# Performance work log

Hardware: AMD Instinct MI355X
Metric: run time of the kernel (lower is better)

## Reference

```python
import jax, jax.numpy as jnp
import numpy as np

N = 100000       # nodes
E = 1000000      # edges
IN = 128         # in_dim
HID = 64         # hid_dim
NET = 4          # n_etypes
STEPS = 5        # n_steps
G = 128          # graphs in batch
LBL = 10         # num_labels


def setup_inputs() -> dict:
    key = jax.random.key(0)
    ks = jax.random.split(key, 20)
    def w(k, shape, fan_in):
        return jax.random.normal(k, shape, jnp.float32) / np.sqrt(fan_in)
    return dict(
        x=jax.random.normal(ks[0], (N, IN), jnp.float32),
        src=jax.random.randint(ks[1], (E,), 0, N),
        dst=jax.random.randint(ks[2], (E,), 0, N),
        etype=jax.random.randint(ks[3], (E,), 0, NET),
        node2graph=jnp.sort(jax.random.randint(ks[4], (N,), 0, G)),
        # linear_in
        W_in=w(ks[5], (HID, IN), IN), b_in=jnp.zeros((HID,), jnp.float32),
        # per-edge-type linears [n_etypes, out, in]
        We=w(ks[6], (NET, HID, HID), HID), be=jnp.zeros((NET, HID), jnp.float32),
        # GRUCell (torch layout: rows = [r; z; n])
        W_ih=w(ks[7], (3 * HID, HID), HID), b_ih=jnp.zeros((3 * HID,), jnp.float32),
        W_hh=w(ks[8], (3 * HID, HID), HID), b_hh=jnp.zeros((3 * HID,), jnp.float32),
        # classifier
        W1=w(ks[9], (HID // 2, HID), HID), b1=jnp.zeros((HID // 2,), jnp.float32),
        W2=w(ks[10], (LBL, HID // 2), HID // 2), b2=jnp.zeros((LBL,), jnp.float32),
    )


def reference(x, W_in, b_in, We, be, W_ih, b_ih, W_hh, b_hh, W1, b1, W2, b2,
              src, dst, etype, node2graph):
    h = x @ W_in.T + b_in                                  # [N, HID]
    for _ in range(STEPS):
        # per-etype linear on node states: trans[e] = h @ We[e].T + be[e]
        trans = jnp.einsum('nd,efd->enf', h, We) + be[:, None, :]  # [NET, N, HID]
        msgs = trans[etype, src]                           # [E, HID] gather per edge
        a = jax.ops.segment_sum(msgs, dst, num_segments=N)  # scatter-add aggregation
        # GRUCell(a, h)
        gi = a @ W_ih.T + b_ih
        gh = h @ W_hh.T + b_hh
        ir, iz, i_n = jnp.split(gi, 3, axis=-1)
        hr, hz, h_n = jnp.split(gh, 3, axis=-1)
        r = jax.nn.sigmoid(ir + hr)
        z = jax.nn.sigmoid(iz + hz)
        n = jnp.tanh(i_n + r * h_n)
        h = (1.0 - z) * n + z * h
    # dgl.mean_nodes: per-graph mean of node states
    cnt = jnp.maximum(jax.ops.segment_sum(jnp.ones((N,), h.dtype), node2graph, num_segments=G), 1.0)
    hg = jax.ops.segment_sum(h, node2graph, num_segments=G) / cnt[:, None]  # [G, HID]
    return jax.nn.relu(hg @ W1.T + b1) @ W2.T + b2         # [G, LBL]
```

## Files before the change

### kernel.cpp

```cpp
#include <hip/hip_runtime.h>
#include <hip/hip_bf16.h>
#include <math.h>

#define N_NODES 100000
#define N_EDGES 1000000
#define IN_DIM 128
#define HID 64
#define NET 4
#define STEPS 5
#define G_GRAPHS 128
#define LBL 10
#define NGRP 6250
#define NGRP_PAD 6256
#define NBKT 1024
#define TILE_E 8192

typedef __attribute__((ext_vector_type(8))) short short8;
typedef __attribute__((ext_vector_type(4))) float f32x4;
typedef unsigned short ushort_t;

__device__ inline ushort_t f2bf(float v) {
    __hip_bfloat16 b = __float2bfloat16(v);
    return __builtin_bit_cast(ushort_t, b);
}
__device__ inline float bf2f(ushort_t u) {
    __hip_bfloat16 b = __builtin_bit_cast(__hip_bfloat16, u);
    return __bfloat162float(b);
}


__global__ void k_pack_b1(const float* __restrict__ We, const float* __restrict__ be,
                          ushort_t* __restrict__ B1, float* __restrict__ bs1) {
    int idx = blockIdx.x * blockDim.x + threadIdx.x;
    if (idx >= 6 * 16 * 4 * 16 * 8) return;
    int j = idx & 7, u = (idx >> 3) & 15, g = (idx >> 7) & 3, ct = (idx >> 9) & 15, s = idx >> 13;
    int m = ct * 16 + u;
    int t = m >> 6, o = m & 63;
    int sk = (s < 2) ? s : (s < 4) ? (s - 2) : (s - 4);
    int k = sk * 32 + g * 8 + j;
    float val = We[t * 4096 + o * 64 + k];
    ushort_t hi = f2bf(val);
    B1[idx] = (s < 4) ? hi : f2bf(val - bf2f(hi));
    if (s == 0 && g == 0 && j == 0) bs1[m] = be[t * 64 + o];
}

__global__ void k_pack_b2(const float* __restrict__ W_ih, const float* __restrict__ b_ih,
                          const float* __restrict__ W_hh, const float* __restrict__ b_hh,
                          ushort_t* __restrict__ B2, float* __restrict__ bg2) {
    int idx = blockIdx.x * blockDim.x + threadIdx.x;
    if (idx >= 12 * 16 * 4 * 16 * 8) return;
    int j = idx & 7, u = (idx >> 3) & 15, g = (idx >> 7) & 3, ct = (idx >> 9) & 15, s = idx >> 13;
    int m = ct * 16 + u;
    int q = m >> 6, gate = (m >> 4) & 3, c = q * 16 + (m & 15);
    int k = (s & 3) * 32 + g * 8 + j;
    float val;
    if (gate == 0)      { int jr = c;        val = (k < 64) ? W_ih[jr * 64 + k] : W_hh[jr * 64 + k - 64]; }
    else if (gate == 1) { int jr = 64 + c;   val = (k < 64) ? W_ih[jr * 64 + k] : W_hh[jr * 64 + k - 64]; }
    else if (gate == 2) { int jr = 128 + c;  val = (k < 64) ? W_ih[jr * 64 + k] : 0.f; }
    else                { int jr = 128 + c;  val = (k < 64) ? 0.f : W_hh[jr * 64 + k - 64]; }
    ushort_t hi = f2bf(val);
    B2[idx] = (s < 8) ? hi : f2bf(val - bf2f(hi));
    if (s == 0 && g == 0 && j == 0) {
        float bv;
        if (gate == 0)      bv = b_ih[c] + b_hh[c];
        else if (gate == 1) bv = b_ih[64 + c] + b_hh[64 + c];
        else if (gate == 2) bv = b_ih[128 + c];
        else                bv = b_hh[128 + c];
        bg2[m] = bv;
    }
}

__global__ void k_pack_bin(const float* __restrict__ W_in, ushort_t* __restrict__ BIN) {
    int idx = blockIdx.x * blockDim.x + threadIdx.x;
    if (idx >= 24576) return;
    int j = idx & 7, lu = (idx >> 3) & 63, ct = (idx >> 9) & 3, s = idx >> 11;
    int g = lu >> 4, u = lu & 15;
    int m = ct * 16 + u;
    int k = (s & 3) * 32 + g * 8 + j;
    float val = W_in[m * 128 + k];
    ushort_t hi = f2bf(val);
    BIN[idx] = (s < 8) ? hi : f2bf(val - bf2f(hi));
}

__global__ __launch_bounds__(256) void k_linear_in(const float* __restrict__ x,
        const ushort_t* __restrict__ BIN, const float* __restrict__ b_in,
        ushort_t* __restrict__ AH) {
    __shared__ float hlds[4][16 * 68];
    int tid = threadIdx.x;
    int lane = tid & 63, wp = tid >> 6;
    int g = lane >> 4, u = lane & 15;
    int grp = blockIdx.x * 4 + wp;
    bool ok = grp < NGRP;
    int row = ok ? (grp * 16 + u) : 0;
    short8 xhi[4], xlo[4];
    #pragma unroll
    for (int ks = 0; ks < 4; ++ks) {
        const float* xp = &x[(size_t)row * 128 + ks * 32 + g * 8];
        float4 v0 = ok ? *(const float4*)xp : make_float4(0.f, 0.f, 0.f, 0.f);
        float4 v1 = ok ? *(const float4*)(xp + 4) : make_float4(0.f, 0.f, 0.f, 0.f);
        float vv[8] = {v0.x, v0.y, v0.z, v0.w, v1.x, v1.y, v1.z, v1.w};
        #pragma unroll
        for (int j = 0; j < 8; ++j) {
            ushort_t hh = f2bf(vv[j]);
            xhi[ks][j] = (short)hh;
            xlo[ks][j] = (short)f2bf(vv[j] - bf2f(hh));
        }
    }
    f32x4 zero = {0.f, 0.f, 0.f, 0.f};
    f32x4 acc[4] = {zero, zero, zero, zero};
    #pragma unroll
    for (int s = 0; s < 12; ++s) {
        int ks = s & 3;
        short8 af = (s < 4) ? xhi[ks] : (s < 8) ? xlo[ks] : xhi[ks];
        #pragma unroll
        for (int ct = 0; ct < 4; ++ct) {
            short8 bf = *(const short8*)&BIN[((size_t)(s * 4 + ct) * 64 + lane) * 8];
            acc[ct] = __builtin_amdgcn_mfma_f32_16x16x32_bf16(af, bf, acc[ct], 0, 0, 0);
        }
    }
    #pragma unroll
    for (int ct = 0; ct < 4; ++ct) {
        float bo = b_in[ct * 16 + u];
        #pragma unroll
        for (int j = 0; j < 4; ++j)
            hlds[wp][(g * 4 + j) * 68 + ct * 16 + u] = acc[ct][j] + bo;
    }
    __syncthreads();
    #pragma unroll
    for (int k = 0; k < 4; ++k) {
        int bi = g + 4 * k;
        short8 ov;
        #pragma unroll
        for (int j = 0; j < 8; ++j) {
            float v = hlds[wp][u * 68 + (bi & 7) * 8 + j];
            ushort_t hh = f2bf(v);
            ov[j] = (bi < 8) ? (short)hh : (short)f2bf(v - bf2f(hh));
        }
        int blk = (bi < 8) ? (8 + bi) : (24 + (bi - 8));
        if (ok) *(short8*)&AH[((size_t)grp * 32 + blk) * 128 + u * 8] = ov;
    }
}


__global__ __launch_bounds__(256) void k_bhist(const int* __restrict__ dst,
        int* __restrict__ bhist) {
    __shared__ int h[NBKT];
    for (int i = threadIdx.x; i < NBKT; i += 256) h[i] = 0;
    __syncthreads();
    int idx = blockIdx.x * 256 + threadIdx.x;
    for (int e = idx; e < N_EDGES; e += 256 * 256) atomicAdd(&h[dst[e] >> 7], 1);
    __syncthreads();
    for (int i = threadIdx.x; i < NBKT; i += 256) {
        int c = h[i];
        if (c) atomicAdd(&bhist[i], c);
    }
}

__global__ __launch_bounds__(1024) void k_bscan(const int* __restrict__ bhist,
        int* __restrict__ bbase, int* __restrict__ bcursor) {
    __shared__ int ts[NBKT];
    int t = threadIdx.x;
    int v = bhist[t];
    ts[t] = v;
    __syncthreads();
    for (int off = 1; off < NBKT; off <<= 1) {
        int u = (t >= off) ? ts[t - off] : 0;
        __syncthreads();
        ts[t] += u;
        __syncthreads();
    }
    int excl = ts[t] - v;
    bbase[t] = excl;
    bcursor[t] = excl;
    if (t == NBKT - 1) bbase[NBKT] = ts[NBKT - 1];
}

__global__ __launch_bounds__(512) void k_bscatter(const int* __restrict__ src,
        const int* __restrict__ dst, const int* __restrict__ et,
        int* __restrict__ bcursor, unsigned int* __restrict__ ebuf) {
    __shared__ int hcnt[NBKT], loff[NBKT], gpos[NBKT], ps[512];
    __shared__ unsigned int stage[TILE_E];
    __shared__ unsigned short sbkt[TILE_E];
    int tid = threadIdx.x;
    int base = blockIdx.x * TILE_E;
    int tilecnt = min(TILE_E, N_EDGES - base);
    for (int i = tid; i < NBKT; i += 512) hcnt[i] = 0;
    __syncthreads();
    #pragma unroll
    for (int k = 0; k < TILE_E / 512; ++k) {
        int e = base + tid + k * 512;
        if (e < N_EDGES) atomicAdd(&hcnt[dst[e] >> 7], 1);
    }
    __syncthreads();
    int c0 = hcnt[tid * 2], c1 = hcnt[tid * 2 + 1];
    ps[tid] = c0 + c1;
    __syncthreads();
    for (int off = 1; off < 512; off <<= 1) {
        int u = (tid >= off) ? ps[tid - off] : 0;
        __syncthreads();
        ps[tid] += u;
        __syncthreads();
    }
    int ex = ps[tid] - (c0 + c1);
    loff[tid * 2] = ex;
    loff[tid * 2 + 1] = ex + c0;
    for (int b = tid; b < NBKT; b += 512) {
        int c = hcnt[b];
        gpos[b] = c ? atomicAdd(&bcursor[b], c) : 0;
    }
    __syncthreads();
    for (int i = tid; i < NBKT; i += 512) hcnt[i] = 0;
    __syncthreads();
    #pragma unroll
    for (int k = 0; k < TILE_E / 512; ++k) {
        int e = base + tid + k * 512;
        if (e < N_EDGES) {
            int d = dst[e];
            int b = d >> 7;
            int r = atomicAdd(&hcnt[b], 1);
            int lp = loff[b] + r;
            stage[lp] = (unsigned int)src[e] | ((unsigned int)et[e] << 20)
                      | ((unsigned int)(d & 127) << 22);
            sbkt[lp] = (unsigned short)b;
        }
    }
    __syncthreads();
    for (int i = tid; i < tilecnt; i += 512) {
        int b = sbkt[i];
        ebuf[gpos[b] + (i - loff[b])] = stage[i];
    }
}

__global__ __launch_bounds__(256) void k_bcsr(const unsigned int* __restrict__ ebuf,
        const int* __restrict__ bbase, int* __restrict__ adj, int* __restrict__ row_ptr) {
    __shared__ int ncnt[128], noff[129], nps[128];
    int b = blockIdx.x;
    int tid = threadIdx.x;
    int ebeg = bbase[b], eend = bbase[b + 1];
    int ecnt = eend - ebeg;
    if (tid < 128) ncnt[tid] = 0;
    __syncthreads();
    for (int i = tid; i < ecnt; i += 256) atomicAdd(&ncnt[(ebuf[ebeg + i] >> 22) & 127], 1);
    __syncthreads();
    int v = (tid < 128) ? ncnt[tid] : 0;
    if (tid < 128) nps[tid] = v;
    __syncthreads();
    for (int off = 1; off < 128; off <<= 1) {
        int u = (tid >= off && tid < 128) ? nps[tid - off] : 0;
        __syncthreads();
        if (tid < 128) nps[tid] += u;
        __syncthreads();
    }
    if (tid < 128) noff[tid] = nps[tid] - v;
    if (tid == 127) noff[128] = nps[127];
    __syncthreads();
    if (tid < 128) ncnt[tid] = 0;
    __syncthreads();
    for (int i = tid; i < ecnt; i += 256) {
        unsigned int p = ebuf[ebeg + i];
        int nl = (p >> 22) & 127;
        int r = atomicAdd(&ncnt[nl], 1);
        adj[ebeg + noff[nl] + r] = (int)(p & 0x3FFFFF);
    }
    for (int i = tid; i <= 128; i += 256) {
        int n = b * 128 + i;
        if (n <= N_NODES) row_ptr[n] = ebeg + noff[i];
    }
}

__global__ __launch_bounds__(512) void k_mm1(const ushort_t* __restrict__ AH,
        const ushort_t* __restrict__ B1, const float* __restrict__ bs1,
        ushort_t* __restrict__ trans) {
    __shared__ ushort_t lds[16896];
    int tid = threadIdx.x;
    size_t gb = (size_t)blockIdx.x * 8;
    #pragma unroll
    for (int it = 0; it < 4; ++it) {
        int f = it * 512 + tid;
        int gl = f >> 8, part = (f >> 7) & 1, inner = f & 127;
        size_t srcp = ((gb + gl) * 32 + (part ? 24 : 8)) * 128 + (size_t)inner * 8;
        *(short8*)&lds[f * 8] = *(const short8*)&AH[srcp];
    }
    __syncthreads();
    int lane = tid & 63, wp = tid >> 6;
    int q = wp & 3, rp = wp >> 2;
    int g = lane >> 4, u = lane & 15;
    int n0 = blockIdx.x * 128;
    f32x4 zero = {0.f, 0.f, 0.f, 0.f};
    f32x4 acc[4][4];
    #pragma unroll
    for (int i = 0; i < 4; ++i)
        #pragma unroll
        for (int j = 0; j < 4; ++j) acc[i][j] = zero;
    #pragma unroll
    for (int s = 0; s < 6; ++s) {
        int part = (s == 2 || s == 3) ? 1 : 0;
        int lb = ((s & 1) ? 4 : 0) + g;
        short8 bfr[4], afr[4];
        #pragma unroll
        for (int ct = 0; ct < 4; ++ct)
            bfr[ct] = *(const short8*)&B1[((size_t)(s * 16 + q * 4 + ct) * 64 + g * 16 + u) * 8];
        #pragma unroll
        for (int rt = 0; rt < 4; ++rt) {
            int gl = rp * 4 + rt;
            afr[rt] = *(const short8*)&lds[((gl * 2 + part) * 8 + lb) * 128 + u * 8];
        }
        #pragma unroll
        for (int rt = 0; rt < 4; ++rt)
            #pragma unroll
            for (int ct = 0; ct < 4; ++ct)
                acc[rt][ct] = __builtin_amdgcn_mfma_f32_16x16x32_bf16(afr[rt], bfr[ct], acc[rt][ct], 0, 0, 0);
    }
    float bsv[4];
    #pragma unroll
    for (int ct = 0; ct < 4; ++ct) bsv[ct] = bs1[q * 64 + ct * 16 + u];
    #pragma unroll
    for (int h = 0; h < 2; ++h) {
        __syncthreads();
        if (rp == h) {
            #pragma unroll
            for (int rt = 0; rt < 4; ++rt)
                #pragma unroll
                for (int ct = 0; ct < 4; ++ct)
                    #pragma unroll
                    for (int j = 0; j < 4; ++j) {
                        int rl = rt * 16 + g * 4 + j;
                        lds[rl * 264 + q * 64 + ct * 16 + u] = f2bf(acc[rt][ct][j] + bsv[ct]);
                    }
        }
        __syncthreads();
        int rl = tid >> 3, seg = tid & 7;
        int n = n0 + h * 64 + rl;
        if (n < N_NODES) {
            #pragma unroll
            for (int i = 0; i < 4; ++i) {
                short8 v = *(const short8*)&lds[rl * 264 + seg * 32 + i * 8];
                *(short8*)&trans[(size_t)n * 256 + seg * 32 + i * 8] = v;
            }
        }
    }
}

__global__ __launch_bounds__(512) void k_mm2(ushort_t* __restrict__ AH,
        const ushort_t* __restrict__ B2, const float* __restrict__ bg2) {
    __shared__ ushort_t lds[32768];
    int tid = threadIdx.x;
    size_t base = (size_t)blockIdx.x * 8 * 4096;
    #pragma unroll
    for (int it = 0; it < 8; ++it) {
        int f = it * 512 + tid;
        *(short8*)&lds[f * 8] = *(const short8*)&AH[base + (size_t)f * 8];
    }
    __syncthreads();
    int lane = tid & 63, wp = tid >> 6;
    int q = wp & 3, rp = wp >> 2;
    int g = lane >> 4, u = lane & 15;
    f32x4 zero = {0.f, 0.f, 0.f, 0.f};
    f32x4 acc[4][4];
    #pragma unroll
    for (int i = 0; i < 4; ++i)
        #pragma unroll
        for (int j = 0; j < 4; ++j) acc[i][j] = zero;
    const int bb2[12] = {0, 4, 8, 12, 16, 20, 24, 28, 0, 4, 8, 12};
    #pragma unroll
    for (int s = 0; s < 12; ++s) {
        short8 bfr[4], afr[4];
        #pragma unroll
        for (int ct = 0; ct < 4; ++ct)
            bfr[ct] = *(const short8*)&B2[((size_t)(s * 16 + q * 4 + ct) * 64 + g * 16 + u) * 8];
        #pragma unroll
        for (int rt = 0; rt < 4; ++rt) {
            int gl = rp * 4 + rt;
            afr[rt] = *(const short8*)&lds[(gl * 32 + bb2[s] + g) * 128 + u * 8];
        }
        #pragma unroll
        for (int rt = 0; rt < 4; ++rt)
            #pragma unroll
            for (int ct = 0; ct < 4; ++ct)
                acc[rt][ct] = __builtin_amdgcn_mfma_f32_16x16x32_bf16(afr[rt], bfr[ct], acc[rt][ct], 0, 0, 0);
    }
    __syncthreads();
    float bgv[4];
    #pragma unroll
    for (int ct = 0; ct < 4; ++ct) bgv[ct] = bg2[q * 64 + ct * 16 + u];
    int hid = q * 16 + u;
    int bhi = 8 + (hid >> 3), blo = 24 + (hid >> 3), el = hid & 7;
    #pragma unroll
    for (int rt = 0; rt < 4; ++rt) {
        int gl = rp * 4 + rt;
        #pragma unroll
        for (int j = 0; j < 4; ++j) {
            int uu = g * 4 + j;
            int shi = (gl * 32 + bhi) * 128 + uu * 8 + el;
            int slo = (gl * 32 + blo) * 128 + uu * 8 + el;
            float ho = bf2f(lds[shi]) + bf2f(lds[slo]);
            float rs  = acc[rt][0][j] + bgv[0];
            float zs  = acc[rt][1][j] + bgv[1];
            float inn = acc[rt][2][j] + bgv[2];
            float hnn = acc[rt][3][j] + bgv[3];
            float r = 1.f / (1.f + __expf(-rs));
            float z = 1.f / (1.f + __expf(-zs));
            float t = inn + r * hnn;
            float e2 = __expf(2.f * t);
            float nn = 1.f - 2.f / (e2 + 1.f);
            float hnew = (1.f - z) * nn + z * ho;
            ushort_t hh = f2bf(hnew);
            lds[shi] = hh;
            lds[slo] = f2bf(hnew - bf2f(hh));
        }
    }
    __syncthreads();
    #pragma unroll
    for (int it = 0; it < 4; ++it) {
        int c = it * 512 + tid;
        int gl = c >> 8, r = c & 255, bi = r >> 4, uu = r & 15;
        int blk = (bi < 8) ? (8 + bi) : (16 + bi);
        int lofs = (gl * 32 + blk) * 128 + uu * 8;
        short8 v = *(const short8*)&lds[lofs];
        *(short8*)&AH[base + (size_t)lofs] = v;
    }
}

__global__ __launch_bounds__(1024) void k_aggregate(const int* __restrict__ row_ptr,
        const int* __restrict__ adj, const ushort_t* __restrict__ trans,
        ushort_t* __restrict__ AH) {
    __shared__ float alds[16 * 72];
    int w = threadIdx.x >> 6, lane = threadIdx.x & 63;
    int grp = blockIdx.x;
    int n = grp * 16 + w;
    int beg = row_ptr[n], end = row_ptr[n + 1];
    float a0 = 0.f, a1 = 0.f, a2 = 0.f, a3 = 0.f;
    int i = beg;
    for (; i + 8 <= end; i += 8) {
        int pk[8];
        #pragma unroll
        for (int t = 0; t < 8; ++t) pk[t] = adj[i + t];
        float v[8];
        #pragma unroll
        for (int t = 0; t < 8; ++t)
            v[t] = bf2f(trans[(size_t)(pk[t] & 0xFFFFF) * 256 + (pk[t] >> 20) * 64 + lane]);
        a0 += v[0] + v[4]; a1 += v[1] + v[5]; a2 += v[2] + v[6]; a3 += v[3] + v[7];
    }
    for (; i + 2 <= end; i += 2) {
        int pk0 = adj[i], pk1 = adj[i + 1];
        a0 += bf2f(trans[(size_t)(pk0 & 0xFFFFF) * 256 + (pk0 >> 20) * 64 + lane]);
        a1 += bf2f(trans[(size_t)(pk1 & 0xFFFFF) * 256 + (pk1 >> 20) * 64 + lane]);
    }
    if (i < end) {
        int pk = adj[i];
        a2 += bf2f(trans[(size_t)(pk & 0xFFFFF) * 256 + (pk >> 20) * 64 + lane]);
    }
    alds[w * 72 + lane] = (a0 + a1) + (a2 + a3);
    __syncthreads();
    if (threadIdx.x < 256) {
        int bi = threadIdx.x >> 4, u = threadIdx.x & 15;
        int b8 = bi & 7;
        bool ishi = bi < 8;
        short8 ov;
        #pragma unroll
        for (int j = 0; j < 8; ++j) {
            float v = alds[u * 72 + b8 * 8 + j];
            ushort_t hh = f2bf(v);
            ov[j] = ishi ? (short)hh : (short)f2bf(v - bf2f(hh));
        }
        *(short8*)&AH[((size_t)grp * 32 + (ishi ? b8 : 16 + b8)) * 128 + u * 8] = ov;
    }
}

__global__ __launch_bounds__(256) void k_pool(const int* __restrict__ n2g,
        const ushort_t* __restrict__ AH, float* __restrict__ hg) {
    int gidx = blockIdx.x;
    int lo = 0, hi = N_NODES;
    while (lo < hi) { int mid = (lo + hi) >> 1; if (n2g[mid] < gidx) lo = mid + 1; else hi = mid; }
    int s = lo;
    hi = N_NODES;
    while (lo < hi) { int mid = (lo + hi) >> 1; if (n2g[mid] < gidx + 1) lo = mid + 1; else hi = mid; }
    int e = lo;
    int w = threadIdx.x >> 6, lane = threadIdx.x & 63;
    int bh = 8 + (lane >> 3), bl = 24 + (lane >> 3), el = lane & 7;
    float sum = 0.f;
    for (int n = s + w; n < e; n += 4) {
        size_t base = (size_t)(n >> 4) * 4096 + (size_t)(n & 15) * 8;
        sum += bf2f(AH[base + bh * 128 + el]) + bf2f(AH[base + bl * 128 + el]);
    }
    __shared__ float red[4][64];
    red[w][lane] = sum;
    __syncthreads();
    if (threadIdx.x < 64) {
        float tot = red[0][lane] + red[1][lane] + red[2][lane] + red[3][lane];
        float cnt = (float)(e - s);
        hg[gidx * 64 + lane] = tot / fmaxf(cnt, 1.f);
    }
}

__global__ __launch_bounds__(64) void k_cls(const float* __restrict__ hg,
        const float* __restrict__ W1, const float* __restrict__ b1,
        const float* __restrict__ W2, const float* __restrict__ b2,
        float* __restrict__ out) {
    int gidx = blockIdx.x;
    __shared__ float v[64];
    __shared__ float m[32];
    v[threadIdx.x] = hg[gidx * 64 + threadIdx.x];
    __syncthreads();
    if (threadIdx.x < 32) {
        float a = b1[threadIdx.x];
        #pragma unroll 8
        for (int k = 0; k < 64; ++k) a = fmaf(v[k], W1[threadIdx.x * 64 + k], a);
        m[threadIdx.x] = fmaxf(a, 0.f);
    }
    __syncthreads();
    if (threadIdx.x < 10) {
        float a = b2[threadIdx.x];
        #pragma unroll
        for (int j = 0; j < 32; ++j) a = fmaf(m[j], W2[threadIdx.x * 32 + j], a);
        out[gidx * 10 + threadIdx.x] = a;
    }
}

extern "C" void kernel_launch(void* const* d_in, const int* in_sizes, int n_in,
                              void* d_out, int out_size, void* d_ws, size_t ws_size,
                              hipStream_t stream) {
    const float* x    = (const float*)d_in[0];
    const int* src    = (const int*)d_in[1];
    const int* dst    = (const int*)d_in[2];
    const int* etype  = (const int*)d_in[3];
    const int* n2g    = (const int*)d_in[4];
    const float* W_in = (const float*)d_in[5];
    const float* b_in = (const float*)d_in[6];
    const float* We   = (const float*)d_in[7];
    const float* be   = (const float*)d_in[8];
    const float* W_ih = (const float*)d_in[9];
    const float* b_ih = (const float*)d_in[10];
    const float* W_hh = (const float*)d_in[11];
    const float* b_hh = (const float*)d_in[12];
    const float* W1   = (const float*)d_in[13];
    const float* b1   = (const float*)d_in[14];
    const float* W2   = (const float*)d_in[15];
    const float* b2   = (const float*)d_in[16];
    float* out = (float*)d_out;

    char* wsb = (char*)d_ws;
    size_t off = 0;
    auto alloc = [&](size_t bytes) -> void* {
        void* p = wsb + off;
        off += (bytes + 255) & ~(size_t)255;
        return p;
    };
    ushort_t* AH      = (ushort_t*)alloc((size_t)NGRP_PAD * 4096 * 2);
    ushort_t* trans   = (ushort_t*)alloc((size_t)N_NODES * 256 * 2);
    int*      adj     = (int*)     alloc((size_t)N_EDGES * 4);
    unsigned int* ebuf = (unsigned int*)alloc((size_t)N_EDGES * 4);
    int*      row_ptr = (int*)     alloc((size_t)(N_NODES + 1) * 4);
    int*      bhist   = (int*)     alloc((size_t)NBKT * 4);
    int*      bbase   = (int*)     alloc((size_t)(NBKT + 1) * 4);
    int*      bcursor = (int*)     alloc((size_t)NBKT * 4);
    ushort_t* B1      = (ushort_t*)alloc((size_t)6 * 16 * 4 * 16 * 8 * 2);
    float*    bs1     = (float*)   alloc(256 * 4);
    ushort_t* B2      = (ushort_t*)alloc((size_t)12 * 16 * 4 * 16 * 8 * 2);
    float*    bg2     = (float*)   alloc(256 * 4);
    ushort_t* BIN     = (ushort_t*)alloc((size_t)24576 * 2);
    float*    hg      = (float*)   alloc(128 * 64 * 4);

    hipMemsetAsync(AH + (size_t)NGRP * 4096, 0, (size_t)(NGRP_PAD - NGRP) * 4096 * 2, stream);

    hipLaunchKernelGGL(k_pack_b1, dim3(192), dim3(256), 0, stream, We, be, B1, bs1);
    hipLaunchKernelGGL(k_pack_b2, dim3(384), dim3(256), 0, stream, W_ih, b_ih, W_hh, b_hh, B2, bg2);
    hipLaunchKernelGGL(k_pack_bin, dim3(96), dim3(256), 0, stream, W_in, BIN);
    hipLaunchKernelGGL(k_linear_in, dim3((NGRP + 3) / 4), dim3(256), 0, stream, x, BIN, b_in, AH);

    hipMemsetAsync(bhist, 0, (size_t)NBKT * 4, stream);
    hipLaunchKernelGGL(k_bhist, dim3(256), dim3(256), 0, stream, dst, bhist);
    hipLaunchKernelGGL(k_bscan, dim3(1), dim3(1024), 0, stream, bhist, bbase, bcursor);
    hipLaunchKernelGGL(k_bscatter, dim3((N_EDGES + TILE_E - 1) / TILE_E), dim3(512), 0, stream,
                       src, dst, etype, bcursor, ebuf);
    hipLaunchKernelGGL(k_bcsr, dim3(NBKT), dim3(256), 0, stream, ebuf, bbase, adj, row_ptr);

    int gblk = NGRP_PAD / 8;
    for (int step = 0; step < STEPS; ++step) {
        hipLaunchKernelGGL(k_mm1, dim3(gblk), dim3(512), 0, stream, AH, B1, bs1, trans);
        hipLaunchKernelGGL(k_aggregate, dim3(NGRP), dim3(1024), 0, stream, row_ptr, adj, trans, AH);
        hipLaunchKernelGGL(k_mm2, dim3(gblk), dim3(512), 0, stream, AH, B2, bg2);
    }
    hipLaunchKernelGGL(k_pool, dim3(G_GRAPHS), dim3(256), 0, stream, n2g, AH, hg);
    hipLaunchKernelGGL(k_cls, dim3(G_GRAPHS), dim3(64), 0, stream, hg, W1, b1, W2, b2, out);
}
```

Baseline: 877.0 us.

## Aggregate raw node states per edge type, then apply edge linear after aggregation

Reorders the math: instead of computing per-etype transformed states for every node and gathering them, each step gathers bf16 hidden rows into four per-etype sums plus counts, then applies the edge-type weights and count-weighted bias with MFMA. The edge gather, edge matmul and GRU matmul are fused into one kernel per step, with ping-pong row-major hidden buffers. This removes the 256-wide trans buffer and two launches per step, and shrinks gather traffic to 64 values per edge. In exchange each block holds four accumulators per lane, uses a large LDS footprint, and gathers only the bf16 high part of h, which lowers precision.

```diff
diff --git a/kernel.cpp b/kernel.cpp
--- a/kernel.cpp
+++ b/kernel.cpp
@@ -29,19 +29,18 @@
 }
 
 
-__global__ void k_pack_b1(const float* __restrict__ We, const float* __restrict__ be,
-                          ushort_t* __restrict__ B1, float* __restrict__ bs1) {
+__global__ void k_pack_bc(const float* __restrict__ We, ushort_t* __restrict__ BC) {
     int idx = blockIdx.x * blockDim.x + threadIdx.x;
-    if (idx >= 6 * 16 * 4 * 16 * 8) return;
-    int j = idx & 7, u = (idx >> 3) & 15, g = (idx >> 7) & 3, ct = (idx >> 9) & 15, s = idx >> 13;
-    int m = ct * 16 + u;
-    int t = m >> 6, o = m & 63;
-    int sk = (s < 2) ? s : (s < 4) ? (s - 2) : (s - 4);
-    int k = sk * 32 + g * 8 + j;
-    float val = We[t * 4096 + o * 64 + k];
+    if (idx >= 24 * 4 * 64 * 8) return;
+    int j = idx & 7, lane = (idx >> 3) & 63, ct = (idx >> 9) & 3, sl = idx >> 11;
+    int g = lane >> 4, u = lane & 15;
+    int p = sl >> 3, ks = sl & 7;
+    int k = ks * 32 + g * 8 + j;
+    int t = k >> 6, d = k & 63;
+    int o = ct * 16 + u;
+    float val = We[t * 4096 + o * 64 + d];
     ushort_t hi = f2bf(val);
-    B1[idx] = (s < 4) ? hi : f2bf(val - bf2f(hi));
-    if (s == 0 && g == 0 && j == 0) bs1[m] = be[t * 64 + o];
+    BC[idx] = (p < 2) ? hi : f2bf(val - bf2f(hi));
 }
 
 __global__ void k_pack_b2(const float* __restrict__ W_ih, const float* __restrict__ b_ih,
@@ -84,7 +83,7 @@
 
 __global__ __launch_bounds__(256) void k_linear_in(const float* __restrict__ x,
         const ushort_t* __restrict__ BIN, const float* __restrict__ b_in,
-        ushort_t* __restrict__ AH) {
+        ushort_t* __restrict__ AH, ushort_t* __restrict__ hrow) {
     __shared__ float hlds[4][16 * 68];
     int tid = threadIdx.x;
     int lane = tid & 63, wp = tid >> 6;
@@ -137,10 +136,13 @@
             ov[j] = (bi < 8) ? (short)hh : (short)f2bf(v - bf2f(hh));
         }
         int blk = (bi < 8) ? (8 + bi) : (24 + (bi - 8));
-        if (ok) *(short8*)&AH[((size_t)grp * 32 + blk) * 128 + u * 8] = ov;
-    }
-}
-
+        if (ok) {
+            *(short8*)&AH[((size_t)grp * 32 + blk) * 128 + u * 8] = ov;
+            if (bi < 8)
+                *(short8*)&hrow[((size_t)(grp * 16 + u)) * 64 + bi * 8] = ov;
+        }
+    }
+}
 
 __global__ __launch_bounds__(256) void k_bhist(const int* __restrict__ dst,
         int* __restrict__ bhist) {
@@ -268,202 +270,207 @@
     }
 }
 
-__global__ __launch_bounds__(512) void k_mm1(const ushort_t* __restrict__ AH,
-        const ushort_t* __restrict__ B1, const float* __restrict__ bs1,
-        ushort_t* __restrict__ trans) {
-    __shared__ ushort_t lds[16896];
-    int tid = threadIdx.x;
-    size_t gb = (size_t)blockIdx.x * 8;
-    #pragma unroll
-    for (int it = 0; it < 4; ++it) {
-        int f = it * 512 + tid;
-        int gl = f >> 8, part = (f >> 7) & 1, inner = f & 127;
-        size_t srcp = ((gb + gl) * 32 + (part ? 24 : 8)) * 128 + (size_t)inner * 8;
-        *(short8*)&lds[f * 8] = *(const short8*)&AH[srcp];
-    }
-    __syncthreads();
-    int lane = tid & 63, wp = tid >> 6;
-    int q = wp & 3, rp = wp >> 2;
+__global__ __launch_bounds__(512) void k_step(const int* __restrict__ row_ptr,
+        const int* __restrict__ adj, const ushort_t* __restrict__ hin,
+        ushort_t* __restrict__ hout, ushort_t* __restrict__ AH,
+        const ushort_t* __restrict__ BC, const float* __restrict__ be,
+        const ushort_t* __restrict__ B2, const float* __restrict__ bg2) {
+    __shared__ float smem[16896];
+    float* aggf = smem;
+    float* cnts = smem + 16640;
+    ushort_t* als  = (ushort_t*)smem;
+    ushort_t* hlds = (ushort_t*)((char*)smem + 17408);
+
+    int tid = threadIdx.x, lane = tid & 63, wp = tid >> 6;
     int g = lane >> 4, u = lane & 15;
-    int n0 = blockIdx.x * 128;
+    int grp0 = blockIdx.x * 4;
+    int nbase = grp0 * 16;
+
+    #pragma unroll 1
+    for (int r = 0; r < 8; ++r) {
+        int nl = wp * 8 + r;
+        int n = nbase + nl;
+        float a0 = 0.f, a1 = 0.f, a2 = 0.f, a3 = 0.f;
+        float c0 = 0.f, c1 = 0.f, c2 = 0.f, c3 = 0.f;
+        if (n < N_NODES) {
+            int beg = row_ptr[n], end = row_ptr[n + 1];
+            int i = beg;
+            for (; i + 4 <= end; i += 4) {
+                int p0 = adj[i], p1 = adj[i + 1], p2 = adj[i + 2], p3 = adj[i + 3];
+                float v0 = bf2f(hin[(size_t)(p0 & 0xFFFFF) * 64 + lane]);
+                float v1 = bf2f(hin[(size_t)(p1 & 0xFFFFF) * 64 + lane]);
+                float v2 = bf2f(hin[(size_t)(p2 & 0xFFFFF) * 64 + lane]);
+                float v3 = bf2f(hin[(size_t)(p3 & 0xFFFFF) * 64 + lane]);
+                int e0 = p0 >> 20, e1 = p1 >> 20, e2 = p2 >> 20, e3 = p3 >> 20;
+                a0 += (e0 == 0) ? v0 : 0.f; a1 += (e0 == 1) ? v0 : 0.f;
+                a2 += (e0 == 2) ? v0 : 0.f; a3 += (e0 == 3) ? v0 : 0.f;
+                a0 += (e1 == 0) ? v1 : 0.f; a1 += (e1 == 1) ? v1 : 0.f;
+                a2 += (e1 == 2) ? v1 : 0.f; a3 += (e1 == 3) ? v1 : 0.f;
+                a0 += (e2 == 0) ? v2 : 0.f; a1 += (e2 == 1) ? v2 : 0.f;
+                a2 += (e2 == 2) ? v2 : 0.f; a3 += (e2 == 3) ? v2 : 0.f;
+                a0 += (e3 == 0) ? v3 : 0.f; a1 += (e3 == 1) ? v3 : 0.f;
+                a2 += (e3 == 2) ? v3 : 0.f; a3 += (e3 == 3) ? v3 : 0.f;
+                c0 += ((e0 == 0) ? 1.f : 0.f) + ((e1 == 0) ? 1.f : 0.f) + ((e2 == 0) ? 1.f : 0.f) + ((e3 == 0) ? 1.f : 0.f);
+                c1 += ((e0 == 1) ? 1.f : 0.f) + ((e1 == 1) ? 1.f : 0.f) + ((e2 == 1) ? 1.f : 0.f) + ((e3 == 1) ? 1.f : 0.f);
+                c2 += ((e0 == 2) ? 1.f : 0.f) + ((e1 == 2) ? 1.f : 0.f) + ((e2 == 2) ? 1.f : 0.f) + ((e3 == 2) ? 1.f : 0.f);
+                c3 += ((e0 == 3) ? 1.f : 0.f) + ((e1 == 3) ? 1.f : 0.f) + ((e2 == 3) ? 1.f : 0.f) + ((e3 == 3) ? 1.f : 0.f);
+            }
+            for (; i < end; ++i) {
+                int pk = adj[i];
+                float v = bf2f(hin[(size_t)(pk & 0xFFFFF) * 64 + lane]);
+                int e = pk >> 20;
+                a0 += (e == 0) ? v : 0.f; a1 += (e == 1) ? v : 0.f;
+                a2 += (e == 2) ? v : 0.f; a3 += (e == 3) ? v : 0.f;
+                c0 += (e == 0) ? 1.f : 0.f; c1 += (e == 1) ? 1.f : 0.f;
+                c2 += (e == 2) ? 1.f : 0.f; c3 += (e == 3) ? 1.f : 0.f;
+            }
+        }
+        aggf[nl * 260 +   0 + lane] = a0;
+        aggf[nl * 260 +  64 + lane] = a1;
+        aggf[nl * 260 + 128 + lane] = a2;
+        aggf[nl * 260 + 192 + lane] = a3;
+        if (lane == 0) {
+            cnts[nl * 4 + 0] = c0; cnts[nl * 4 + 1] = c1;
+            cnts[nl * 4 + 2] = c2; cnts[nl * 4 + 3] = c3;
+        }
+    }
+    __syncthreads();
+
+    int rp1 = wp >> 1, cq = wp & 1;
     f32x4 zero = {0.f, 0.f, 0.f, 0.f};
-    f32x4 acc[4][4];
-    #pragma unroll
-    for (int i = 0; i < 4; ++i)
-        #pragma unroll
-        for (int j = 0; j < 4; ++j) acc[i][j] = zero;
-    #pragma unroll
-    for (int s = 0; s < 6; ++s) {
-        int part = (s == 2 || s == 3) ? 1 : 0;
-        int lb = ((s & 1) ? 4 : 0) + g;
-        short8 bfr[4], afr[4];
+    f32x4 acc1[2] = {zero, zero};
+    #pragma unroll
+    for (int ks = 0; ks < 8; ++ks) {
+        const float* ap = &aggf[(rp1 * 16 + u) * 260 + ks * 32 + g * 8];
+        f32x4 x0 = *(const f32x4*)ap;
+        f32x4 x1 = *(const f32x4*)(ap + 4);
+        short8 ahi, alo;
+        #pragma unroll
+        for (int j = 0; j < 4; ++j) {
+            ushort_t hh = f2bf(x0[j]);
+            ahi[j] = (short)hh; alo[j] = (short)f2bf(x0[j] - bf2f(hh));
+            ushort_t hh2 = f2bf(x1[j]);
+            ahi[4 + j] = (short)hh2; alo[4 + j] = (short)f2bf(x1[j] - bf2f(hh2));
+        }
+        #pragma unroll
+        for (int p = 0; p < 3; ++p) {
+            short8 af = (p == 1) ? alo : ahi;
+            #pragma unroll
+            for (int ct = 0; ct < 2; ++ct) {
+                short8 bf = *(const short8*)&BC[((size_t)((p * 8 + ks) * 4 + cq * 2 + ct) * 64 + lane) * 8];
+                acc1[ct] = __builtin_amdgcn_mfma_f32_16x16x32_bf16(af, bf, acc1[ct], 0, 0, 0);
+            }
+        }
+    }
+    __syncthreads();
+
+    {
+        float beL[2][4];
+        #pragma unroll
+        for (int ct = 0; ct < 2; ++ct)
+            #pragma unroll
+            for (int t = 0; t < 4; ++t)
+                beL[ct][t] = be[t * 64 + cq * 32 + ct * 16 + u];
+        #pragma unroll
+        for (int j = 0; j < 4; ++j) {
+            int row = rp1 * 16 + g * 4 + j;
+            f32x4 cn = *(const f32x4*)&cnts[row * 4];
+            #pragma unroll
+            for (int ct = 0; ct < 2; ++ct) {
+                float v = acc1[ct][j] + cn[0] * beL[ct][0] + cn[1] * beL[ct][1]
+                                      + cn[2] * beL[ct][2] + cn[3] * beL[ct][3];
+                int col = cq * 32 + ct * 16 + u;
+                ushort_t hh = f2bf(v);
+                als[row * 136 + col] = hh;
+                als[row * 136 + 64 + col] = f2bf(v - bf2f(hh));
+            }
+        }
+    }
+    #pragma unroll
+    for (int it = 0; it < 2; ++it) {
+        int c = it * 512 + tid;
+        int gl = c >> 8, r = c & 255, bi = r >> 4, uu = r & 15;
+        int blk = (bi < 8) ? (8 + bi) : (24 + (bi - 8));
+        *(short8*)&hlds[((gl * 16 + bi) * 16 + uu) * 8] =
+            *(const short8*)&AH[((size_t)(grp0 + gl) * 32 + blk) * 128 + uu * 8];
+    }
+    __syncthreads();
+
+    int q = wp & 3, rp2 = wp >> 2;
+    f32x4 acc2[2][4];
+    #pragma unroll
+    for (int i = 0; i < 2; ++i)
+        #pragma unroll
+        for (int j = 0; j < 4; ++j) acc2[i][j] = zero;
+    #pragma unroll
+    for (int s = 0; s < 12; ++s) {
+        int p2 = s >> 2, ks2 = s & 3;
+        short8 bfr[4], afr[2];
         #pragma unroll
         for (int ct = 0; ct < 4; ++ct)
-            bfr[ct] = *(const short8*)&B1[((size_t)(s * 16 + q * 4 + ct) * 64 + g * 16 + u) * 8];
-        #pragma unroll
-        for (int rt = 0; rt < 4; ++rt) {
-            int gl = rp * 4 + rt;
-            afr[rt] = *(const short8*)&lds[((gl * 2 + part) * 8 + lb) * 128 + u * 8];
-        }
-        #pragma unroll
-        for (int rt = 0; rt < 4; ++rt)
+            bfr[ct] = *(const short8*)&B2[((size_t)(s * 16 + q * 4 + ct) * 64 + g * 16 + u) * 8];
+        #pragma unroll
+        for (int rt = 0; rt < 2; ++rt) {
+            int row = rp2 * 32 + rt * 16 + u;
+            if (ks2 < 2) {
+                int base = ((p2 == 1) ? 64 : 0) + ks2 * 32 + g * 8;
+                afr[rt] = *(const short8*)&als[row * 136 + base];
+            } else {
+                int part = (p2 == 1) ? 1 : 0;
+                int gl = rp2 * 2 + rt;
+                int bi = part * 8 + (ks2 - 2) * 4 + g;
+                afr[rt] = *(const short8*)&hlds[((gl * 16 + bi) * 16 + u) * 8];
+            }
+        }
+        #pragma unroll
+        for (int rt = 0; rt < 2; ++rt)
             #pragma unroll
             for (int ct = 0; ct < 4; ++ct)
-                acc[rt][ct] = __builtin_amdgcn_mfma_f32_16x16x32_bf16(afr[rt], bfr[ct], acc[rt][ct], 0, 0, 0);
-    }
-    float bsv[4];
-    #pragma unroll
-    for (int ct = 0; ct < 4; ++ct) bsv[ct] = bs1[q * 64 + ct * 16 + u];
-    #pragma unroll
-    for (int h = 0; h < 2; ++h) {
-        __syncthreads();
-        if (rp == h) {
+                acc2[rt][ct] = __builtin_amdgcn_mfma_f32_16x16x32_bf16(afr[rt], bfr[ct], acc2[rt][ct], 0, 0, 0);
+    }
+    __syncthreads();
+
+    {
+        float bgv[4];
+        #pragma unroll
+        for (int ct = 0; ct < 4; ++ct) bgv[ct] = bg2[q * 64 + ct * 16 + u];
+        int hid = q * 16 + u;
+        #pragma unroll
+        for (int rt = 0; rt < 2; ++rt) {
+            int gl = rp2 * 2 + rt;
             #pragma unroll
-            for (int rt = 0; rt < 4; ++rt)
-                #pragma unroll
-                for (int ct = 0; ct < 4; ++ct)
-                    #pragma unroll
-                    for (int j = 0; j < 4; ++j) {
-                        int rl = rt * 16 + g * 4 + j;
-                        lds[rl * 264 + q * 64 + ct * 16 + u] = f2bf(acc[rt][ct][j] + bsv[ct]);
-                    }
-        }
-        __syncthreads();
-        int rl = tid >> 3, seg = tid & 7;
-        int n = n0 + h * 64 + rl;
-        if (n < N_NODES) {
-            #pragma unroll
-            for (int i = 0; i < 4; ++i) {
-                short8 v = *(const short8*)&lds[rl * 264 + seg * 32 + i * 8];
-                *(short8*)&trans[(size_t)n * 256 + seg * 32 + i * 8] = v;
+            for (int j = 0; j < 4; ++j) {
+                int uu = g * 4 + j;
+                int shi = ((gl * 16 + (hid >> 3)) * 16 + uu) * 8 + (hid & 7);
+                int slo = ((gl * 16 + 8 + (hid >> 3)) * 16 + uu) * 8 + (hid & 7);
+                float ho = bf2f(hlds[shi]) + bf2f(hlds[slo]);
+                float rs  = acc2[rt][0][j] + bgv[0];
+                float zs  = acc2[rt][1][j] + bgv[1];
+                float inn = acc2[rt][2][j] + bgv[2];
+                float hnn = acc2[rt][3][j] + bgv[3];
+                float rr = 1.f / (1.f + __expf(-rs));
+                float zz = 1.f / (1.f + __expf(-zs));
+                float t = inn + rr * hnn;
+                float e2 = __expf(2.f * t);
+                float nn = 1.f - 2.f / (e2 + 1.f);
+                float hnew = (1.f - zz) * nn + zz * ho;
+                ushort_t hh = f2bf(hnew);
+                hlds[shi] = hh;
+                hlds[slo] = f2bf(hnew - bf2f(hh));
             }
         }
     }
-}
-
-__global__ __launch_bounds__(512) void k_mm2(ushort_t* __restrict__ AH,
-        const ushort_t* __restrict__ B2, const float* __restrict__ bg2) {
-    __shared__ ushort_t lds[32768];
-    int tid = threadIdx.x;
-    size_t base = (size_t)blockIdx.x * 8 * 4096;
-    #pragma unroll
-    for (int it = 0; it < 8; ++it) {
-        int f = it * 512 + tid;
-        *(short8*)&lds[f * 8] = *(const short8*)&AH[base + (size_t)f * 8];
-    }
-    __syncthreads();
-    int lane = tid & 63, wp = tid >> 6;
-    int q = wp & 3, rp = wp >> 2;
-    int g = lane >> 4, u = lane & 15;
-    f32x4 zero = {0.f, 0.f, 0.f, 0.f};
-    f32x4 acc[4][4];
-    #pragma unroll
-    for (int i = 0; i < 4; ++i)
-        #pragma unroll
-        for (int j = 0; j < 4; ++j) acc[i][j] = zero;
-    const int bb2[12] = {0, 4, 8, 12, 16, 20, 24, 28, 0, 4, 8, 12};
-    #pragma unroll
-    for (int s = 0; s < 12; ++s) {
-        short8 bfr[4], afr[4];
-        #pragma unroll
-        for (int ct = 0; ct < 4; ++ct)
-            bfr[ct] = *(const short8*)&B2[((size_t)(s * 16 + q * 4 + ct) * 64 + g * 16 + u) * 8];
-        #pragma unroll
-        for (int rt = 0; rt < 4; ++rt) {
-            int gl = rp * 4 + rt;
-            afr[rt] = *(const short8*)&lds[(gl * 32 + bb2[s] + g) * 128 + u * 8];
-        }
-        #pragma unroll
-        for (int rt = 0; rt < 4; ++rt)
-            #pragma unroll
-            for (int ct = 0; ct < 4; ++ct)
-                acc[rt][ct] = __builtin_amdgcn_mfma_f32_16x16x32_bf16(afr[rt], bfr[ct], acc[rt][ct], 0, 0, 0);
-    }
-    __syncthreads();
-    float bgv[4];
-    #pragma unroll
-    for (int ct = 0; ct < 4; ++ct) bgv[ct] = bg2[q * 64 + ct * 16 + u];
-    int hid = q * 16 + u;
-    int bhi = 8 + (hid >> 3), blo = 24 + (hid >> 3), el = hid & 7;
-    #pragma unroll
-    for (int rt = 0; rt < 4; ++rt) {
-        int gl = rp * 4 + rt;
-        #pragma unroll
-        for (int j = 0; j < 4; ++j) {
-            int uu = g * 4 + j;
-            int shi = (gl * 32 + bhi) * 128 + uu * 8 + el;
-            int slo = (gl * 32 + blo) * 128 + uu * 8 + el;
-            float ho = bf2f(lds[shi]) + bf2f(lds[slo]);
-            float rs  = acc[rt][0][j] + bgv[0];
-            float zs  = acc[rt][1][j] + bgv[1];
-            float inn = acc[rt][2][j] + bgv[2];
-            float hnn = acc[rt][3][j] + bgv[3];
-            float r = 1.f / (1.f + __expf(-rs));
-            float z = 1.f / (1.f + __expf(-zs));
-            float t = inn + r * hnn;
-            float e2 = __expf(2.f * t);
-            float nn = 1.f - 2.f / (e2 + 1.f);
-            float hnew = (1.f - z) * nn + z * ho;
-            ushort_t hh = f2bf(hnew);
-            lds[shi] = hh;
-            lds[slo] = f2bf(hnew - bf2f(hh));
-        }
-    }
-    __syncthreads();
-    #pragma unroll
-    for (int it = 0; it < 4; ++it) {
+    __syncthreads();
+
+    #pragma unroll
+    for (int it = 0; it < 2; ++it) {
         int c = it * 512 + tid;
         int gl = c >> 8, r = c & 255, bi = r >> 4, uu = r & 15;
-        int blk = (bi < 8) ? (8 + bi) : (16 + bi);
-        int lofs = (gl * 32 + blk) * 128 + uu * 8;
-        short8 v = *(const short8*)&lds[lofs];
-        *(short8*)&AH[base + (size_t)lofs] = v;
-    }
-}
-
-__global__ __launch_bounds__(1024) void k_aggregate(const int* __restrict__ row_ptr,
-        const int* __restrict__ adj, const ushort_t* __restrict__ trans,
-        ushort_t* __restrict__ AH) {
-    __shared__ float alds[16 * 72];
-    int w = threadIdx.x >> 6, lane = threadIdx.x & 63;
-    int grp = blockIdx.x;
-    int n = grp * 16 + w;
-    int beg = row_ptr[n], end = row_ptr[n + 1];
-    float a0 = 0.f, a1 = 0.f, a2 = 0.f, a3 = 0.f;
-    int i = beg;
-    for (; i + 8 <= end; i += 8) {
-        int pk[8];
-        #pragma unroll
-        for (int t = 0; t < 8; ++t) pk[t] = adj[i + t];
-        float v[8];
-        #pragma unroll
-        for (int t = 0; t < 8; ++t)
-            v[t] = bf2f(trans[(size_t)(pk[t] & 0xFFFFF) * 256 + (pk[t] >> 20) * 64 + lane]);
-        a0 += v[0] + v[4]; a1 += v[1] + v[5]; a2 += v[2] + v[6]; a3 += v[3] + v[7];
-    }
-    for (; i + 2 <= end; i += 2) {
-        int pk0 = adj[i], pk1 = adj[i + 1];
-        a0 += bf2f(trans[(size_t)(pk0 & 0xFFFFF) * 256 + (pk0 >> 20) * 64 + lane]);
-        a1 += bf2f(trans[(size_t)(pk1 & 0xFFFFF) * 256 + (pk1 >> 20) * 64 + lane]);
-    }
-    if (i < end) {
-        int pk = adj[i];
-        a2 += bf2f(trans[(size_t)(pk & 0xFFFFF) * 256 + (pk >> 20) * 64 + lane]);
-    }
-    alds[w * 72 + lane] = (a0 + a1) + (a2 + a3);
-    __syncthreads();
-    if (threadIdx.x < 256) {
-        int bi = threadIdx.x >> 4, u = threadIdx.x & 15;
-        int b8 = bi & 7;
-        bool ishi = bi < 8;
-        short8 ov;
-        #pragma unroll
-        for (int j = 0; j < 8; ++j) {
-            float v = alds[u * 72 + b8 * 8 + j];
-            ushort_t hh = f2bf(v);
-            ov[j] = ishi ? (short)hh : (short)f2bf(v - bf2f(hh));
-        }
-        *(short8*)&AH[((size_t)grp * 32 + (ishi ? b8 : 16 + b8)) * 128 + u * 8] = ov;
+        short8 v = *(const short8*)&hlds[((gl * 16 + bi) * 16 + uu) * 8];
+        int blk = (bi < 8) ? (8 + bi) : (24 + (bi - 8));
+        *(short8*)&AH[((size_t)(grp0 + gl) * 32 + blk) * 128 + uu * 8] = v;
+        if (bi < 8)
+            *(short8*)&hout[((size_t)((grp0 + gl) * 16 + uu)) * 64 + bi * 8] = v;
     }
 }
 
@@ -547,26 +554,26 @@
         return p;
     };
     ushort_t* AH      = (ushort_t*)alloc((size_t)NGRP_PAD * 4096 * 2);
-    ushort_t* trans   = (ushort_t*)alloc((size_t)N_NODES * 256 * 2);
+    ushort_t* hrowA   = (ushort_t*)alloc((size_t)NGRP_PAD * 16 * 64 * 2);
+    ushort_t* hrowB   = (ushort_t*)alloc((size_t)NGRP_PAD * 16 * 64 * 2);
     int*      adj     = (int*)     alloc((size_t)N_EDGES * 4);
     unsigned int* ebuf = (unsigned int*)alloc((size_t)N_EDGES * 4);
     int*      row_ptr = (int*)     alloc((size_t)(N_NODES + 1) * 4);
     int*      bhist   = (int*)     alloc((size_t)NBKT * 4);
     int*      bbase   = (int*)     alloc((size_t)(NBKT + 1) * 4);
     int*      bcursor = (int*)     alloc((size_t)NBKT * 4);
-    ushort_t* B1      = (ushort_t*)alloc((size_t)6 * 16 * 4 * 16 * 8 * 2);
-    float*    bs1     = (float*)   alloc(256 * 4);
     ushort_t* B2      = (ushort_t*)alloc((size_t)12 * 16 * 4 * 16 * 8 * 2);
     float*    bg2     = (float*)   alloc(256 * 4);
     ushort_t* BIN     = (ushort_t*)alloc((size_t)24576 * 2);
+    ushort_t* BC      = (ushort_t*)alloc((size_t)24 * 4 * 64 * 8 * 2);
     float*    hg      = (float*)   alloc(128 * 64 * 4);
 
     hipMemsetAsync(AH + (size_t)NGRP * 4096, 0, (size_t)(NGRP_PAD - NGRP) * 4096 * 2, stream);
 
-    hipLaunchKernelGGL(k_pack_b1, dim3(192), dim3(256), 0, stream, We, be, B1, bs1);
     hipLaunchKernelGGL(k_pack_b2, dim3(384), dim3(256), 0, stream, W_ih, b_ih, W_hh, b_hh, B2, bg2);
     hipLaunchKernelGGL(k_pack_bin, dim3(96), dim3(256), 0, stream, W_in, BIN);
-    hipLaunchKernelGGL(k_linear_in, dim3((NGRP + 3) / 4), dim3(256), 0, stream, x, BIN, b_in, AH);
+    hipLaunchKernelGGL(k_pack_bc, dim3(192), dim3(256), 0, stream, We, BC);
+    hipLaunchKernelGGL(k_linear_in, dim3((NGRP + 3) / 4), dim3(256), 0, stream, x, BIN, b_in, AH, hrowA);
 
     hipMemsetAsync(bhist, 0, (size_t)NBKT * 4, stream);
     hipLaunchKernelGGL(k_bhist, dim3(256), dim3(256), 0, stream, dst, bhist);
@@ -575,11 +582,12 @@
                        src, dst, etype, bcursor, ebuf);
     hipLaunchKernelGGL(k_bcsr, dim3(NBKT), dim3(256), 0, stream, ebuf, bbase, adj, row_ptr);
 
-    int gblk = NGRP_PAD / 8;
+    int sblk = NGRP_PAD / 4;
     for (int step = 0; step < STEPS; ++step) {
-        hipLaunchKernelGGL(k_mm1, dim3(gblk), dim3(512), 0, stream, AH, B1, bs1, trans);
-        hipLaunchKernelGGL(k_aggregate, dim3(NGRP), dim3(1024), 0, stream, row_ptr, adj, trans, AH);
-        hipLaunchKernelGGL(k_mm2, dim3(gblk), dim3(512), 0, stream, AH, B2, bg2);
+        const ushort_t* hin = (step & 1) ? hrowB : hrowA;
+        ushort_t* hout      = (step & 1) ? hrowA : hrowB;
+        hipLaunchKernelGGL(k_step, dim3(sblk), dim3(512), 0, stream,
+                           row_ptr, adj, hin, hout, AH, BC, be, B2, bg2);
     }
     hipLaunchKernelGGL(k_pool, dim3(G_GRAPHS), dim3(256), 0, stream, n2g, AH, hg);
     hipLaunchKernelGGL(k_cls, dim3(G_GRAPHS), dim3(64), 0, stream, hg, W1, b1, W2, b2, out);
```

New measurement: 841.4 us. -4.1%, faster.
